# Optimization experiments

Measured on AMD Instinct MI355X. Metric: run time of the kernel, lower is better.

Reference implementation:

```python
import jax, jax.numpy as jnp
import numpy as np

H = 768
NH = 12
DH = H // NH  # 64


def setup_inputs() -> dict:
    key = jax.random.key(0)
    ks = jax.random.split(key, 20)
    s = 1.0 / np.sqrt(H)
    def lin(k, din, dout):
        kw, kb = jax.random.split(k)
        W = jax.random.uniform(kw, (din, dout), jnp.float32, -s, s)
        b = jax.random.uniform(kb, (dout,), jnp.float32, -s, s)
        return W, b
    Wq, bq = lin(ks[0], H, H)
    Wk, bk = lin(ks[1], H, H)
    Wv, bv = lin(ks[2], H, H)
    Wt, bt = lin(ks[3], H, H)
    Wi, bi = lin(ks[4], H, H)
    W1, b1 = lin(ks[5], H, H)
    W2, b2 = lin(ks[6], H, 1)
    text = jax.random.normal(ks[7], (8, 64, H), jnp.float32)
    image = jax.random.normal(ks[8], (8, 197, H), jnp.float32)
    return dict(text=text, image=image, Wq=Wq, bq=bq, Wk=Wk, bk=bk, Wv=Wv, bv=bv,
                Wt=Wt, bt=bt, Wi=Wi, bi=bi, W1=W1, b1=b1, W2=W2, b2=b2)


def reference(text, image, Wq, bq, Wk, bk, Wv, bv, Wt, bt, Wi, bi, W1, b1, W2, b2):
    bsz, t_len, _ = text.shape
    i_len = image.shape[1]
    # relevance gate MLP on broadcast product
    text_emb = text @ Wt + bt          # [b, t, H]
    image_emb = image @ Wi + bi        # [b, i, H]
    rel = text_emb[:, :, None, :] * image_emb[:, None, :, :]  # [b, t, i, H]
    rel = jax.nn.relu(rel @ W1 + b1)
    gate = jax.nn.sigmoid(rel @ W2 + b2)  # [b, t, i, 1]
    gate = gate.reshape(bsz, 1, t_len, i_len)
    # cross-attention
    def heads(x, L):
        return x.reshape(bsz, L, NH, DH).transpose(0, 2, 1, 3)  # [b, h, L, dh]
    q = heads(text @ Wq + bq, t_len)
    k = heads(image @ Wk + bk, i_len)
    v = heads(image @ Wv + bv, i_len)
    scores = jnp.einsum('bhtd,bhid->bhti', q, k) / np.sqrt(DH)
    probs = jax.nn.softmax(scores, axis=-1) * gate   # [b, h, t, i]
    ctx = jnp.einsum('bhti,bhid->bhtd', probs, v)    # [b, h, t, dh]
    return ctx.transpose(0, 2, 1, 3).reshape(bsz, t_len, H)
```

## Files before the change

### kernel.cpp

```cpp
#include <hip/hip_runtime.h>
#include <stdint.h>

#define HD 768
#define NHEADS 12
#define DHEAD 64
#define BATCH 8
#define TLEN 64
#define ILEN 197
#define NPAIRS 100864
#define MTILES 394

typedef __attribute__((ext_vector_type(8))) short short8;
typedef __attribute__((ext_vector_type(4))) float f32x4;

__device__ __forceinline__ short f2bf(float x) {
    union { float f; uint32_t u; } v; v.f = x;
    uint32_t r = v.u + 0x7FFFu + ((v.u >> 16) & 1u);
    return (short)(r >> 16);
}
__device__ __forceinline__ float bf2f(short s) {
    union { uint32_t u; float f; } v; v.u = ((uint32_t)(unsigned short)s) << 16;
    return v.f;
}
__device__ __forceinline__ void gll16(const void* g, void* l) {
    __builtin_amdgcn_global_load_lds(
        (const __attribute__((address_space(1))) unsigned int*)g,
        (__attribute__((address_space(3))) unsigned int*)l, 16, 0, 0);
}

__global__ __launch_bounds__(256) void prep_weights(
    const float* __restrict__ Wq, const float* __restrict__ Wk,
    const float* __restrict__ Wv, const float* __restrict__ Wt,
    const float* __restrict__ Wi, const float* __restrict__ W1,
    short* __restrict__ W5s, short* __restrict__ W1Bs)
{
    __shared__ float tile[64][65];
    int bx = blockIdx.x;
    int tid = threadIdx.x;
    if (bx >= 720) {
        int idx = bx - 720;
        int pn = idx / 12, kt = idx - pn * 12;
        int c = tid;
        int j = pn * 256 + c;
        char* dst = (char*)W1Bs + (size_t)idx * 32768 + c * 128;
        int swz = (c & 7) << 4;
#pragma unroll
        for (int kg = 0; kg < 8; ++kg) {
            short8 o;
#pragma unroll
            for (int e = 0; e < 8; ++e)
                o[e] = f2bf(W1[(size_t)(kt * 64 + kg * 8 + e) * HD + j]);
            *(short8*)(dst + ((kg * 16) ^ swz)) = o;
        }
        return;
    }
    int seg = bx / 144, ti = bx - seg * 144;
    const float* src = (seg == 0) ? Wt : (seg == 1) ? Wq : (seg == 2) ? Wi
                     : (seg == 3) ? Wk : Wv;
    int kt = ti / 12, ntile = ti - kt * 12;
#pragma unroll
    for (int pass = 0; pass < 16; ++pass) {
        int idx = pass * 256 + tid;
        int kk = idx >> 6, nn = idx & 63;
        tile[kk][nn] = src[(size_t)(kt * 64 + kk) * HD + ntile * 64 + nn];
    }
    __syncthreads();
    size_t base = ((size_t)(seg * 12 + ntile) * 12 + kt) * 8192;
#pragma unroll
    for (int pass = 0; pass < 16; ++pass) {
        int idx = pass * 256 + tid;
        int col = idx >> 6, kloc = idx & 63;
        float x = tile[kloc][col];
        short h = f2bf(x);
        short lw = f2bf(x - bf2f(h));
        int sidx = (col * 64 + kloc) ^ ((col & 7) << 3);
        W5s[base + sidx] = h;
        W5s[base + 4096 + sidx] = lw;
    }
}

__global__ __launch_bounds__(256, 1) void proj_kernel(
    const float* __restrict__ X, int M,
    const short* __restrict__ W5s, int segbase,
    const float* __restrict__ bias0, const float* __restrict__ bias1,
    const float* __restrict__ bias2,
    float* __restrict__ out0, float* __restrict__ out1, float* __restrict__ out2)
{
    __shared__ __align__(16) short Bs[2][8192];
    int tid = threadIdx.x;
    int l = tid & 63, w = tid >> 6;
    int lo = l & 15, grp = l >> 4;
    int y = blockIdx.y;
    int segl = y / 12, ntile = y - segl * 12;
    int seg = segbase + segl;
    const char* wsrc = (const char*)W5s + (size_t)((seg * 12 + ntile) * 12) * 16384;
    {
        const char* s = wsrc + w * 4096 + l * 16;
        char* d = (char*)&Bs[0][0] + w * 4096;
        gll16(s, d); gll16(s + 1024, d + 1024);
        gll16(s + 2048, d + 2048); gll16(s + 3072, d + 3072);
    }
    int arow = blockIdx.x * 64 + w * 16 + lo;
    bool aok = arow < M;
    const float* xrow = X + (size_t)(aok ? arow : 0) * HD;
    short8 ah[24], al[24];
#pragma unroll
    for (int kc = 0; kc < 24; ++kc) {
        int kb = kc * 32 + grp * 8;
        float4 xa = {0.f, 0.f, 0.f, 0.f}, xb = {0.f, 0.f, 0.f, 0.f};
        if (aok) { xa = *(const float4*)(xrow + kb); xb = *(const float4*)(xrow + kb + 4); }
        float xs[8] = {xa.x, xa.y, xa.z, xa.w, xb.x, xb.y, xb.z, xb.w};
#pragma unroll
        for (int e = 0; e < 8; ++e) {
            short hh = f2bf(xs[e]);
            ah[kc][e] = hh;
            al[kc][e] = f2bf(xs[e] - bf2f(hh));
        }
    }
    __syncthreads();

    f32x4 acc[4];
    f32x4 z4 = {0.f, 0.f, 0.f, 0.f};
#pragma unroll
    for (int js = 0; js < 4; ++js) acc[js] = z4;

#pragma unroll
    for (int kk = 0; kk < 12; ++kk) {
        const short* buf = &Bs[kk & 1][0];
        if (kk < 11) {
            const char* s = wsrc + (size_t)(kk + 1) * 16384 + w * 4096 + l * 16;
            char* d = (char*)&Bs[(kk + 1) & 1][0] + w * 4096;
            gll16(s, d); gll16(s + 1024, d + 1024);
            gll16(s + 2048, d + 2048); gll16(s + 3072, d + 3072);
            asm volatile("s_waitcnt vmcnt(4)" ::: "memory");
        } else {
            asm volatile("s_waitcnt vmcnt(0)" ::: "memory");
        }
        __builtin_amdgcn_s_barrier();
        asm volatile("" ::: "memory");
#pragma unroll
        for (int js = 0; js < 4; ++js) {
            int col = js * 16 + lo;
            int base = col * 64;
            int sw = (col & 7) << 3;
#pragma unroll
            for (int kcl = 0; kcl < 2; ++kcl) {
                int idx = (base + kcl * 32 + grp * 8) ^ sw;
                short8 bh = *(const short8*)&buf[idx];
                short8 bl = *(const short8*)&buf[4096 + idx];
                int kc = kk * 2 + kcl;
                acc[js] = __builtin_amdgcn_mfma_f32_16x16x32_bf16(ah[kc], bh, acc[js], 0, 0, 0);
                acc[js] = __builtin_amdgcn_mfma_f32_16x16x32_bf16(ah[kc], bl, acc[js], 0, 0, 0);
                acc[js] = __builtin_amdgcn_mfma_f32_16x16x32_bf16(al[kc], bh, acc[js], 0, 0, 0);
            }
        }
        asm volatile("s_waitcnt lgkmcnt(0)" ::: "memory");
        __builtin_amdgcn_s_barrier();
        asm volatile("" ::: "memory");
    }
    const float* bp = (segl == 0) ? bias0 : (segl == 1) ? bias1 : bias2;
    float* op = (segl == 0) ? out0 : (segl == 1) ? out1 : out2;
#pragma unroll
    for (int js = 0; js < 4; ++js) {
        int cc = ntile * 64 + js * 16 + lo;
        float bvv = bp[cc];
#pragma unroll
        for (int r = 0; r < 4; ++r) {
            int orow = blockIdx.x * 64 + w * 16 + grp * 4 + r;
            if (orow < M) op[(size_t)orow * HD + cc] = acc[js][r] + bvv;
        }
    }
}

__global__ __launch_bounds__(256) void build_a(
    const float* __restrict__ te, const float* __restrict__ ie,
    short* __restrict__ As, int mstart)
{
    int bx = blockIdx.x;
    int m_l = bx / 12, kt = bx - m_l * 12;
    int tid = threadIdx.x;
    int p = (mstart + m_l) * 256 + tid;
    int b = p / 12608; int rr = p - b * 12608;
    int t = rr / 197;  int i = rr - t * 197;
    const float* tp = te + (size_t)(b * 64 + t) * HD + kt * 64;
    const float* ip = ie + (size_t)(b * 197 + i) * HD + kt * 64;
    char* dst = (char*)As + ((size_t)(m_l * 12 + kt) * 32768) + tid * 128;
    int swz = (tid & 7) << 4;
#pragma unroll
    for (int kg = 0; kg < 8; ++kg) {
        float4 xa = *(const float4*)(ip + kg * 8);
        float4 xb = *(const float4*)(ip + kg * 8 + 4);
        float4 ta = *(const float4*)(tp + kg * 8);
        float4 tb = *(const float4*)(tp + kg * 8 + 4);
        short8 o;
        o[0] = f2bf(xa.x * ta.x); o[1] = f2bf(xa.y * ta.y);
        o[2] = f2bf(xa.z * ta.z); o[3] = f2bf(xa.w * ta.w);
        o[4] = f2bf(xb.x * tb.x); o[5] = f2bf(xb.y * tb.y);
        o[6] = f2bf(xb.z * tb.z); o[7] = f2bf(xb.w * tb.w);
        *(short8*)(dst + ((kg * 16) ^ swz)) = o;
    }
}

__global__ __launch_bounds__(512, 2) void gate_gemm(
    const short* __restrict__ As, const short* __restrict__ W1Bs,
    const float* __restrict__ b1, const float* __restrict__ W2,
    float* __restrict__ plg, int mstart)
{
    __shared__ __align__(16) char lds[131072];
    int tid = threadIdx.x;
    int lane = tid & 63, wid = tid >> 6;
    int lo = lane & 15, grp = lane >> 4;
    int wr = wid >> 2, wc = wid & 3;
    int bx0 = blockIdx.x;
    int nwg = gridDim.x;
    int qq = nwg >> 3, rr8 = nwg & 7;
    int xcd = bx0 & 7;
    int logical = (xcd < rr8 ? xcd * (qq + 1) : rr8 * (qq + 1) + (xcd - rr8) * qq)
                + (bx0 >> 3);
    int m_l = logical / 3, pn = logical - m_l * 3;

    const char* Ag = (const char*)As + (size_t)m_l * 12 * 32768;
    const char* Bg = (const char*)W1Bs + (size_t)pn * 12 * 32768;

    {
        gll16(Ag + tid * 16,          lds + tid * 16);
        gll16(Ag + 8192 + tid * 16,   lds + 8192 + tid * 16);
        gll16(Ag + 16384 + tid * 16,  lds + 16384 + tid * 16);
        gll16(Ag + 24576 + tid * 16,  lds + 24576 + tid * 16);
        gll16(Bg + tid * 16,          lds + 65536 + tid * 16);
        gll16(Bg + 8192 + tid * 16,   lds + 65536 + 8192 + tid * 16);
        gll16(Bg + 16384 + tid * 16,  lds + 65536 + 16384 + tid * 16);
        gll16(Bg + 24576 + tid * 16,  lds + 65536 + 24576 + tid * 16);
    }
    asm volatile("s_waitcnt vmcnt(0)" ::: "memory");
    __builtin_amdgcn_s_barrier();
    asm volatile("" ::: "memory");

    f32x4 acc[8][4];
    f32x4 z4 = {0.f, 0.f, 0.f, 0.f};
#pragma unroll
    for (int rt = 0; rt < 8; ++rt)
#pragma unroll
        for (int ct = 0; ct < 4; ++ct) acc[rt][ct] = z4;
    int swz = (lo & 7) << 4;

    for (int kt = 0; kt < 12; ++kt) {
        int par = kt & 1, npar = par ^ 1;
        int aoff = par * 32768;
        int boff = 65536 + par * 32768;
        bool more = kt < 11;
        const char* Aun = Ag + (size_t)(kt + 1) * 32768;
        const char* Bun = Bg + (size_t)(kt + 1) * 32768;
        int dA = npar * 32768, dB = 65536 + npar * 32768;

        short8 bfr[4][2];
#pragma unroll
        for (int q = 0; q < 4; ++q) {
            short8 af[2][2];
#pragma unroll
            for (int i2 = 0; i2 < 2; ++i2) {
                int r = wr * 128 + (2 * q + i2) * 16 + lo;
#pragma unroll
                for (int ks = 0; ks < 2; ++ks)
                    af[i2][ks] = *(const short8*)(lds + aoff + r * 128 + ((ks * 64 + grp * 16) ^ swz));
            }
            if (q == 0) {
#pragma unroll
                for (int ct = 0; ct < 4; ++ct) {
                    int c = wc * 64 + ct * 16 + lo;
#pragma unroll
                    for (int ks = 0; ks < 2; ++ks)
                        bfr[ct][ks] = *(const short8*)(lds + boff + c * 128 + ((ks * 64 + grp * 16) ^ swz));
                }
            }
            if (more) {
                if (q < 2) {
                    gll16(Aun + (size_t)(q * 2) * 8192 + tid * 16,
                          lds + dA + (q * 2) * 8192 + tid * 16);
                    gll16(Aun + (size_t)(q * 2 + 1) * 8192 + tid * 16,
                          lds + dA + (q * 2 + 1) * 8192 + tid * 16);
                } else {
                    gll16(Bun + (size_t)((q - 2) * 2) * 8192 + tid * 16,
                          lds + dB + ((q - 2) * 2) * 8192 + tid * 16);
                    gll16(Bun + (size_t)((q - 2) * 2 + 1) * 8192 + tid * 16,
                          lds + dB + ((q - 2) * 2 + 1) * 8192 + tid * 16);
                }
            }
            asm volatile("" ::: "memory");
            __builtin_amdgcn_s_barrier();
            asm volatile("s_waitcnt lgkmcnt(0)" ::: "memory");
            __builtin_amdgcn_sched_barrier(0);
            __builtin_amdgcn_s_setprio(1);
#pragma unroll
            for (int i2 = 0; i2 < 2; ++i2)
#pragma unroll
                for (int ct = 0; ct < 4; ++ct)
#pragma unroll
                    for (int ks = 0; ks < 2; ++ks)
                        acc[2 * q + i2][ct] = __builtin_amdgcn_mfma_f32_16x16x32_bf16(
                            af[i2][ks], bfr[ct][ks], acc[2 * q + i2][ct], 0, 0, 0);
            __builtin_amdgcn_s_setprio(0);
            if (q == 3) {
                asm volatile("s_waitcnt vmcnt(0)" ::: "memory");
            }
            __builtin_amdgcn_s_barrier();
            asm volatile("" ::: "memory");
        }
    }

    float b1v[4], w2v[4];
#pragma unroll
    for (int ct = 0; ct < 4; ++ct) {
        int j = pn * 256 + wc * 64 + ct * 16 + lo;
        b1v[ct] = b1[j]; w2v[ct] = W2[j];
    }
    float pl[8][4];
#pragma unroll
    for (int rt = 0; rt < 8; ++rt)
#pragma unroll
        for (int r = 0; r < 4; ++r) {
            float s = 0.f;
#pragma unroll
            for (int ct = 0; ct < 4; ++ct)
                s += fmaxf(acc[rt][ct][r] + b1v[ct], 0.f) * w2v[ct];
            pl[rt][r] = s;
        }
#pragma unroll
    for (int msk = 1; msk <= 8; msk <<= 1)
#pragma unroll
        for (int rt = 0; rt < 8; ++rt)
#pragma unroll
            for (int r = 0; r < 4; ++r)
                pl[rt][r] += __shfl_xor(pl[rt][r], msk);

    __syncthreads();
    float* red = (float*)lds;
    if (lo == 0) {
#pragma unroll
        for (int rt = 0; rt < 8; ++rt)
#pragma unroll
            for (int r = 0; r < 4; ++r)
                red[wid * 128 + rt * 16 + grp * 4 + r] = pl[rt][r];
    }
    __syncthreads();
    if (tid < 256) {
        int wr_ = tid >> 7, rl = tid & 127;
        float s = red[(wr_ * 4 + 0) * 128 + rl] + red[(wr_ * 4 + 1) * 128 + rl]
                + red[(wr_ * 4 + 2) * 128 + rl] + red[(wr_ * 4 + 3) * 128 + rl];
        plg[(size_t)pn * NPAIRS + (size_t)(mstart + m_l) * 256 + tid] = s;
    }
}

__global__ __launch_bounds__(256) void gate_fin(
    const float* __restrict__ plg, const float* __restrict__ b2,
    float* __restrict__ gateb)
{
    int idx = blockIdx.x * 256 + threadIdx.x;
    if (idx < NPAIRS) {
        float s = plg[idx] + plg[NPAIRS + idx] + plg[2 * NPAIRS + idx] + b2[0];
        gateb[idx] = 1.f / (1.f + __expf(-s));
    }
}

__global__ __launch_bounds__(256) void attn_kernel(
    const float* __restrict__ q, const float* __restrict__ k,
    const float* __restrict__ v, const float* __restrict__ gate,
    float* __restrict__ out)
{
    __shared__ float k_s[ILEN * 65];
    __shared__ float p_s[4][ILEN][4];
    int bx = blockIdx.x;
    int tq = bx & 3;
    int h = (bx >> 2) % NHEADS;
    int b = bx / (4 * NHEADS);
    int tid = threadIdx.x;
    for (int idx = tid; idx < ILEN * DHEAD; idx += 256) {
        int i = idx >> 6, d = idx & 63;
        k_s[i * 65 + d] = k[(size_t)(b * ILEN + i) * HD + h * DHEAD + d];
    }
    __syncthreads();

    int l = tid & 63, w = tid >> 6;
    int tbase = tq * 16 + w * 4;

    for (int tt = 0; tt < 4; ++tt) {
        int t = tbase + tt;
        float qv = q[(size_t)(b * 64 + t) * HD + h * DHEAD + l];
        float s0 = 0.f, s1 = 0.f, s2 = 0.f, s3 = 0.f;
        int i0 = l, i1 = 64 + l, i2 = 128 + l;
        int i3c = (192 + l < ILEN) ? 192 + l : 0;
        for (int d = 0; d < 64; ++d) {
            float qd = __shfl(qv, d);
            s0 += qd * k_s[i0 * 65 + d];
            s1 += qd * k_s[i1 * 65 + d];
            s2 += qd * k_s[i2 * 65 + d];
            s3 += qd * k_s[i3c * 65 + d];
        }
        float sc[4] = {s0, s1, s2, s3};
        float m = -3.0e38f;
#pragma unroll
        for (int rep = 0; rep < 4; ++rep) {
            int i = rep * 64 + l;
            sc[rep] = (i < ILEN) ? sc[rep] * 0.125f : -3.0e38f;
            m = fmaxf(m, sc[rep]);
        }
        for (int mask = 32; mask >= 1; mask >>= 1) m = fmaxf(m, __shfl_xor(m, mask));
        float sum = 0.f;
#pragma unroll
        for (int rep = 0; rep < 4; ++rep) {
            float e = __expf(sc[rep] - m);
            sc[rep] = e;
            sum += e;
        }
        for (int mask = 32; mask >= 1; mask >>= 1) sum += __shfl_xor(sum, mask);
        float inv = 1.f / sum;
        const float* grow = gate + (size_t)(b * 64 + t) * ILEN;
#pragma unroll
        for (int rep = 0; rep < 4; ++rep) {
            int i = rep * 64 + l;
            if (i < ILEN) p_s[w][i][tt] = sc[rep] * inv * grow[i];
        }
    }

    float ctx[4] = {0.f, 0.f, 0.f, 0.f};
    const float* vbase = v + (size_t)(b * ILEN) * HD + h * DHEAD + l;
#pragma unroll 4
    for (int i = 0; i < ILEN; ++i) {
        float vv = vbase[(size_t)i * HD];
        float4 p4 = *(const float4*)&p_s[w][i][0];
        ctx[0] += p4.x * vv;
        ctx[1] += p4.y * vv;
        ctx[2] += p4.z * vv;
        ctx[3] += p4.w * vv;
    }
#pragma unroll
    for (int tt = 0; tt < 4; ++tt)
        out[(size_t)(b * 64 + tbase + tt) * HD + h * DHEAD + l] = ctx[tt];
}

extern "C" void kernel_launch(void* const* d_in, const int* in_sizes, int n_in,
                              void* d_out, int out_size, void* d_ws, size_t ws_size,
                              hipStream_t stream)
{
    const float* text  = (const float*)d_in[0];
    const float* image = (const float*)d_in[1];
    const float* Wq = (const float*)d_in[2];
    const float* bq = (const float*)d_in[3];
    const float* Wk = (const float*)d_in[4];
    const float* bk = (const float*)d_in[5];
    const float* Wv = (const float*)d_in[6];
    const float* bv = (const float*)d_in[7];
    const float* Wt = (const float*)d_in[8];
    const float* bt = (const float*)d_in[9];
    const float* Wi = (const float*)d_in[10];
    const float* bi = (const float*)d_in[11];
    const float* W1 = (const float*)d_in[12];
    const float* b1 = (const float*)d_in[13];
    const float* W2 = (const float*)d_in[14];
    const float* b2 = (const float*)d_in[15];
    float* out = (float*)d_out;

    char* ws = (char*)d_ws;
    size_t off = 0;
    auto carve = [&](size_t bytes) -> void* {
        void* p = (void*)(ws + off);
        off += (bytes + 255) & ~(size_t)255;
        return p;
    };
    short* W5s  = (short*)carve((size_t)5 * 144 * 8192 * 2);
    short* W1Bs = (short*)carve((size_t)36 * 32768);
    float* te    = (float*)carve((size_t)512 * 768 * 4);
    float* qb    = (float*)carve((size_t)512 * 768 * 4);
    float* ieb   = (float*)carve((size_t)1576 * 768 * 4);
    float* kb    = (float*)carve((size_t)1576 * 768 * 4);
    float* vb    = (float*)carve((size_t)1576 * 768 * 4);
    float* gateb = (float*)carve((size_t)NPAIRS * 4);
    float* plg   = (float*)carve((size_t)3 * NPAIRS * 4);

    size_t per_m = (size_t)12 * 32768;
    size_t avail = (ws_size > off) ? (ws_size - off) : 0;
    int stripe = (int)(avail / per_m);
    if (stripe > MTILES) stripe = MTILES;
    if (stripe < 1) stripe = 1;
    short* As = (short*)(ws + off);
    int nst = (MTILES + stripe - 1) / stripe;

    hipLaunchKernelGGL(prep_weights, dim3(756), dim3(256), 0, stream,
                       Wq, Wk, Wv, Wt, Wi, W1, W5s, W1Bs);
    hipLaunchKernelGGL(proj_kernel, dim3(8, 24), dim3(256), 0, stream,
                       text, 512, W5s, 0, bt, bq, (const float*)nullptr,
                       te, qb, (float*)nullptr);
    hipLaunchKernelGGL(proj_kernel, dim3(25, 36), dim3(256), 0, stream,
                       image, 1576, W5s, 2, bi, bk, bv,
                       ieb, kb, vb);
    for (int s = 0; s < nst; ++s) {
        int m0 = s * stripe;
        int mc = (MTILES - m0 < stripe) ? (MTILES - m0) : stripe;
        hipLaunchKernelGGL(build_a, dim3(mc * 12), dim3(256), 0, stream,
                           te, ieb, As, m0);
        hipLaunchKernelGGL(gate_gemm, dim3(mc * 3), dim3(512), 0, stream,
                           As, W1Bs, b1, W2, plg, m0);
    }
    hipLaunchKernelGGL(gate_fin, dim3((NPAIRS + 255) / 256), dim3(256), 0, stream,
                       plg, b2, gateb);
    hipLaunchKernelGGL(attn_kernel, dim3(BATCH * NHEADS * 4), dim3(256), 0, stream,
                       qb, kb, vb, gateb, out);
}
```

Baseline: 346.6 us.

## Retile gate GEMM to 192-wide N and triple-buffer A with one barrier per k-step

The gate GEMM's N tile shrinks from 256 to 192 columns, so there are four column blocks per M tile instead of three. The pre-packed W1 layout, the grid size and the partial-logit buffer (now four partial sums added in gate_fin) are all adjusted to match. The k-loop changes from double-buffering with eight barriers per k-tile to triple-buffered A and double-buffered B tiles. It uses explicit vmcnt waits and a single barrier per k-tile, so loads are issued two stages ahead. This aims to cut barrier stalls, improve overlap of loads with MFMA work, and spread more workgroups across CUs, at the cost of larger LDS use (144KB) and a slightly lower MFMA-to-load ratio per block.

```diff
diff --git a/kernel.cpp b/kernel.cpp
--- a/kernel.cpp
+++ b/kernel.cpp
@@ -41,16 +41,18 @@
         int idx = bx - 720;
         int pn = idx / 12, kt = idx - pn * 12;
         int c = tid;
-        int j = pn * 256 + c;
-        char* dst = (char*)W1Bs + (size_t)idx * 32768 + c * 128;
-        int swz = (c & 7) << 4;
-#pragma unroll
-        for (int kg = 0; kg < 8; ++kg) {
-            short8 o;
-#pragma unroll
-            for (int e = 0; e < 8; ++e)
-                o[e] = f2bf(W1[(size_t)(kt * 64 + kg * 8 + e) * HD + j]);
-            *(short8*)(dst + ((kg * 16) ^ swz)) = o;
+        if (c < 192) {
+            int j = pn * 192 + c;
+            char* dst = (char*)W1Bs + (size_t)idx * 24576 + c * 128;
+            int swz = (c & 7) << 4;
+#pragma unroll
+            for (int kg = 0; kg < 8; ++kg) {
+                short8 o;
+#pragma unroll
+                for (int e = 0; e < 8; ++e)
+                    o[e] = f2bf(W1[(size_t)(kt * 64 + kg * 8 + e) * HD + j]);
+                *(short8*)(dst + ((kg * 16) ^ swz)) = o;
+            }
         }
         return;
     }
@@ -206,7 +208,7 @@
     const float* __restrict__ b1, const float* __restrict__ W2,
     float* __restrict__ plg, int mstart)
 {
-    __shared__ __align__(16) char lds[131072];
+    __shared__ __align__(16) char lds[147456];
     int tid = threadIdx.x;
     int lane = tid & 63, wid = tid >> 6;
     int lo = lane & 15, grp = lane >> 4;
@@ -217,43 +219,51 @@
     int xcd = bx0 & 7;
     int logical = (xcd < rr8 ? xcd * (qq + 1) : rr8 * (qq + 1) + (xcd - rr8) * qq)
                 + (bx0 >> 3);
-    int m_l = logical / 3, pn = logical - m_l * 3;
+    int m_l = logical >> 2, pn = logical & 3;
 
     const char* Ag = (const char*)As + (size_t)m_l * 12 * 32768;
-    const char* Bg = (const char*)W1Bs + (size_t)pn * 12 * 32768;
-
-    {
-        gll16(Ag + tid * 16,          lds + tid * 16);
-        gll16(Ag + 8192 + tid * 16,   lds + 8192 + tid * 16);
-        gll16(Ag + 16384 + tid * 16,  lds + 16384 + tid * 16);
-        gll16(Ag + 24576 + tid * 16,  lds + 24576 + tid * 16);
-        gll16(Bg + tid * 16,          lds + 65536 + tid * 16);
-        gll16(Bg + 8192 + tid * 16,   lds + 65536 + 8192 + tid * 16);
-        gll16(Bg + 16384 + tid * 16,  lds + 65536 + 16384 + tid * 16);
-        gll16(Bg + 24576 + tid * 16,  lds + 65536 + 24576 + tid * 16);
-    }
-    asm volatile("s_waitcnt vmcnt(0)" ::: "memory");
-    __builtin_amdgcn_s_barrier();
-    asm volatile("" ::: "memory");
-
-    f32x4 acc[8][4];
+    const char* Bg = (const char*)W1Bs + (size_t)pn * 12 * 24576;
+
+    auto stageA = [&](int t) {
+        const char* s = Ag + (size_t)t * 32768 + tid * 16;
+        char* d = lds + (t % 3) * 32768 + tid * 16;
+        gll16(s, d); gll16(s + 8192, d + 8192);
+        gll16(s + 16384, d + 16384); gll16(s + 24576, d + 24576);
+    };
+    auto stageB = [&](int t) {
+        const char* s = Bg + (size_t)t * 24576 + tid * 16;
+        char* d = lds + 98304 + (t & 1) * 24576 + tid * 16;
+        gll16(s, d); gll16(s + 8192, d + 8192); gll16(s + 16384, d + 16384);
+    };
+    stageB(0); stageA(0); stageB(1); stageA(1);
+
+    f32x4 acc[8][3];
     f32x4 z4 = {0.f, 0.f, 0.f, 0.f};
 #pragma unroll
     for (int rt = 0; rt < 8; ++rt)
 #pragma unroll
-        for (int ct = 0; ct < 4; ++ct) acc[rt][ct] = z4;
+        for (int ct = 0; ct < 3; ++ct) acc[rt][ct] = z4;
     int swz = (lo & 7) << 4;
 
     for (int kt = 0; kt < 12; ++kt) {
-        int par = kt & 1, npar = par ^ 1;
-        int aoff = par * 32768;
-        int boff = 65536 + par * 32768;
-        bool more = kt < 11;
-        const char* Aun = Ag + (size_t)(kt + 1) * 32768;
-        const char* Bun = Bg + (size_t)(kt + 1) * 32768;
-        int dA = npar * 32768, dB = 65536 + npar * 32768;
-
-        short8 bfr[4][2];
+        if (kt == 0)       asm volatile("s_waitcnt vmcnt(7)" ::: "memory");
+        else if (kt == 11) asm volatile("s_waitcnt vmcnt(0)" ::: "memory");
+        else               asm volatile("s_waitcnt vmcnt(4)" ::: "memory");
+        __builtin_amdgcn_s_barrier();
+        asm volatile("" ::: "memory");
+        if (kt >= 1 && kt + 1 < 12) stageB(kt + 1);
+        if (kt + 2 < 12)            stageA(kt + 2);
+
+        int aoff = (kt % 3) * 32768;
+        int boff = 98304 + (kt & 1) * 24576;
+        short8 bfr[3][2];
+#pragma unroll
+        for (int ct = 0; ct < 3; ++ct) {
+            int c = wc * 48 + ct * 16 + lo;
+#pragma unroll
+            for (int ks = 0; ks < 2; ++ks)
+                bfr[ct][ks] = *(const short8*)(lds + boff + c * 128 + ((ks * 64 + grp * 16) ^ swz));
+        }
 #pragma unroll
         for (int q = 0; q < 4; ++q) {
             short8 af[2][2];
@@ -264,54 +274,23 @@
                 for (int ks = 0; ks < 2; ++ks)
                     af[i2][ks] = *(const short8*)(lds + aoff + r * 128 + ((ks * 64 + grp * 16) ^ swz));
             }
-            if (q == 0) {
-#pragma unroll
-                for (int ct = 0; ct < 4; ++ct) {
-                    int c = wc * 64 + ct * 16 + lo;
-#pragma unroll
-                    for (int ks = 0; ks < 2; ++ks)
-                        bfr[ct][ks] = *(const short8*)(lds + boff + c * 128 + ((ks * 64 + grp * 16) ^ swz));
-                }
-            }
-            if (more) {
-                if (q < 2) {
-                    gll16(Aun + (size_t)(q * 2) * 8192 + tid * 16,
-                          lds + dA + (q * 2) * 8192 + tid * 16);
-                    gll16(Aun + (size_t)(q * 2 + 1) * 8192 + tid * 16,
-                          lds + dA + (q * 2 + 1) * 8192 + tid * 16);
-                } else {
-                    gll16(Bun + (size_t)((q - 2) * 2) * 8192 + tid * 16,
-                          lds + dB + ((q - 2) * 2) * 8192 + tid * 16);
-                    gll16(Bun + (size_t)((q - 2) * 2 + 1) * 8192 + tid * 16,
-                          lds + dB + ((q - 2) * 2 + 1) * 8192 + tid * 16);
-                }
-            }
-            asm volatile("" ::: "memory");
-            __builtin_amdgcn_s_barrier();
-            asm volatile("s_waitcnt lgkmcnt(0)" ::: "memory");
-            __builtin_amdgcn_sched_barrier(0);
             __builtin_amdgcn_s_setprio(1);
 #pragma unroll
             for (int i2 = 0; i2 < 2; ++i2)
 #pragma unroll
-                for (int ct = 0; ct < 4; ++ct)
+                for (int ct = 0; ct < 3; ++ct)
 #pragma unroll
                     for (int ks = 0; ks < 2; ++ks)
                         acc[2 * q + i2][ct] = __builtin_amdgcn_mfma_f32_16x16x32_bf16(
                             af[i2][ks], bfr[ct][ks], acc[2 * q + i2][ct], 0, 0, 0);
             __builtin_amdgcn_s_setprio(0);
-            if (q == 3) {
-                asm volatile("s_waitcnt vmcnt(0)" ::: "memory");
-            }
-            __builtin_amdgcn_s_barrier();
-            asm volatile("" ::: "memory");
-        }
-    }
-
-    float b1v[4], w2v[4];
-#pragma unroll
-    for (int ct = 0; ct < 4; ++ct) {
-        int j = pn * 256 + wc * 64 + ct * 16 + lo;
+        }
+    }
+
+    float b1v[3], w2v[3];
+#pragma unroll
+    for (int ct = 0; ct < 3; ++ct) {
+        int j = pn * 192 + wc * 48 + ct * 16 + lo;
         b1v[ct] = b1[j]; w2v[ct] = W2[j];
     }
     float pl[8][4];
@@ -321,7 +300,7 @@
         for (int r = 0; r < 4; ++r) {
             float s = 0.f;
 #pragma unroll
-            for (int ct = 0; ct < 4; ++ct)
+            for (int ct = 0; ct < 3; ++ct)
                 s += fmaxf(acc[rt][ct][r] + b1v[ct], 0.f) * w2v[ct];
             pl[rt][r] = s;
         }
@@ -357,7 +336,8 @@
 {
     int idx = blockIdx.x * 256 + threadIdx.x;
     if (idx < NPAIRS) {
-        float s = plg[idx] + plg[NPAIRS + idx] + plg[2 * NPAIRS + idx] + b2[0];
+        float s = plg[idx] + plg[NPAIRS + idx] + plg[2 * NPAIRS + idx]
+                + plg[3 * NPAIRS + idx] + b2[0];
         gateb[idx] = 1.f / (1.f + __expf(-s));
     }
 }
@@ -468,14 +448,14 @@
         return p;
     };
     short* W5s  = (short*)carve((size_t)5 * 144 * 8192 * 2);
-    short* W1Bs = (short*)carve((size_t)36 * 32768);
+    short* W1Bs = (short*)carve((size_t)48 * 24576);
     float* te    = (float*)carve((size_t)512 * 768 * 4);
     float* qb    = (float*)carve((size_t)512 * 768 * 4);
     float* ieb   = (float*)carve((size_t)1576 * 768 * 4);
     float* kb    = (float*)carve((size_t)1576 * 768 * 4);
     float* vb    = (float*)carve((size_t)1576 * 768 * 4);
     float* gateb = (float*)carve((size_t)NPAIRS * 4);
-    float* plg   = (float*)carve((size_t)3 * NPAIRS * 4);
+    float* plg   = (float*)carve((size_t)4 * NPAIRS * 4);
 
     size_t per_m = (size_t)12 * 32768;
     size_t avail = (ws_size > off) ? (ws_size - off) : 0;
@@ -485,7 +465,7 @@
     short* As = (short*)(ws + off);
     int nst = (MTILES + stripe - 1) / stripe;
 
-    hipLaunchKernelGGL(prep_weights, dim3(756), dim3(256), 0, stream,
+    hipLaunchKernelGGL(prep_weights, dim3(768), dim3(256), 0, stream,
                        Wq, Wk, Wv, Wt, Wi, W1, W5s, W1Bs);
     hipLaunchKernelGGL(proj_kernel, dim3(8, 24), dim3(256), 0, stream,
                        text, 512, W5s, 0, bt, bq, (const float*)nullptr,
@@ -498,7 +478,7 @@
         int mc = (MTILES - m0 < stripe) ? (MTILES - m0) : stripe;
         hipLaunchKernelGGL(build_a, dim3(mc * 12), dim3(256), 0, stream,
                            te, ieb, As, m0);
-        hipLaunchKernelGGL(gate_gemm, dim3(mc * 3), dim3(512), 0, stream,
+        hipLaunchKernelGGL(gate_gemm, dim3(mc * 4), dim3(512), 0, stream,
                            As, W1Bs, b1, W2, plg, m0);
     }
     hipLaunchKernelGGL(gate_fin, dim3((NPAIRS + 255) / 256), dim3(256), 0, stream,
```

New measurement: 361.7 us. 1.04x slower.

## Fuse relevance-product A-tile construction into gate GEMM and drop striped launches

Applied to the files above, without the earlier changes.

Removes the separate build_a kernel and its bf16 staging buffer. Each gate_gemm block now builds its own A tile in LDS from the text and image embeddings (elementwise product, then bf16 conversion), for the next K step, while the MFMAs for the current step run. This avoids writing and re-reading roughly 150MB of intermediate A data and the striped launch loop. In exchange, the fp32 embeddings are re-read three times (once per N-tile block), the per-q barriers are replaced by one barrier per K step, and the A construction uses plain vector global loads instead of direct-to-LDS loads, so latency overlap depends on the compiler's scheduling.

```diff
diff --git a/kernel.cpp b/kernel.cpp
--- a/kernel.cpp
+++ b/kernel.cpp
@@ -172,39 +172,10 @@
     }
 }
 
-__global__ __launch_bounds__(256) void build_a(
+__global__ __launch_bounds__(512, 2) void gate_gemm(
     const float* __restrict__ te, const float* __restrict__ ie,
-    short* __restrict__ As, int mstart)
-{
-    int bx = blockIdx.x;
-    int m_l = bx / 12, kt = bx - m_l * 12;
-    int tid = threadIdx.x;
-    int p = (mstart + m_l) * 256 + tid;
-    int b = p / 12608; int rr = p - b * 12608;
-    int t = rr / 197;  int i = rr - t * 197;
-    const float* tp = te + (size_t)(b * 64 + t) * HD + kt * 64;
-    const float* ip = ie + (size_t)(b * 197 + i) * HD + kt * 64;
-    char* dst = (char*)As + ((size_t)(m_l * 12 + kt) * 32768) + tid * 128;
-    int swz = (tid & 7) << 4;
-#pragma unroll
-    for (int kg = 0; kg < 8; ++kg) {
-        float4 xa = *(const float4*)(ip + kg * 8);
-        float4 xb = *(const float4*)(ip + kg * 8 + 4);
-        float4 ta = *(const float4*)(tp + kg * 8);
-        float4 tb = *(const float4*)(tp + kg * 8 + 4);
-        short8 o;
-        o[0] = f2bf(xa.x * ta.x); o[1] = f2bf(xa.y * ta.y);
-        o[2] = f2bf(xa.z * ta.z); o[3] = f2bf(xa.w * ta.w);
-        o[4] = f2bf(xb.x * tb.x); o[5] = f2bf(xb.y * tb.y);
-        o[6] = f2bf(xb.z * tb.z); o[7] = f2bf(xb.w * tb.w);
-        *(short8*)(dst + ((kg * 16) ^ swz)) = o;
-    }
-}
-
-__global__ __launch_bounds__(512, 2) void gate_gemm(
-    const short* __restrict__ As, const short* __restrict__ W1Bs,
-    const float* __restrict__ b1, const float* __restrict__ W2,
-    float* __restrict__ plg, int mstart)
+    const short* __restrict__ W1Bs, const float* __restrict__ b1,
+    const float* __restrict__ W2, float* __restrict__ plg)
 {
     __shared__ __align__(16) char lds[131072];
     int tid = threadIdx.x;
@@ -219,20 +190,47 @@
                 + (bx0 >> 3);
     int m_l = logical / 3, pn = logical - m_l * 3;
 
-    const char* Ag = (const char*)As + (size_t)m_l * 12 * 32768;
     const char* Bg = (const char*)W1Bs + (size_t)pn * 12 * 32768;
 
+    int crow = wid * 32 + (lane >> 1);
+    int ckh  = lane & 1;
     {
-        gll16(Ag + tid * 16,          lds + tid * 16);
-        gll16(Ag + 8192 + tid * 16,   lds + 8192 + tid * 16);
-        gll16(Ag + 16384 + tid * 16,  lds + 16384 + tid * 16);
-        gll16(Ag + 24576 + tid * 16,  lds + 24576 + tid * 16);
-        gll16(Bg + tid * 16,          lds + 65536 + tid * 16);
-        gll16(Bg + 8192 + tid * 16,   lds + 65536 + 8192 + tid * 16);
-        gll16(Bg + 16384 + tid * 16,  lds + 65536 + 16384 + tid * 16);
-        gll16(Bg + 24576 + tid * 16,  lds + 65536 + 24576 + tid * 16);
-    }
-    asm volatile("s_waitcnt vmcnt(0)" ::: "memory");
+    }
+    int cp = m_l * 256 + crow;
+    int cb = cp / 12608; int crr = cp - cb * 12608;
+    int ct_ = crr / 197; int ci = crr - ct_ * 197;
+    const float* ctp = te + (size_t)(cb * 64 + ct_) * HD + ckh * 32;
+    const float* cip = ie + (size_t)(cb * 197 + ci) * HD + ckh * 32;
+    int cawz = (crow & 7) << 4;
+    int ckg0 = ckh * 4;
+
+    auto constructA = [&](int t, int par) {
+        const float* tpk = ctp + (size_t)t * 64;
+        const float* ipk = cip + (size_t)t * 64;
+        char* ab = lds + par * 32768 + crow * 128;
+#pragma unroll
+        for (int g = 0; g < 4; ++g) {
+            float4 ta = *(const float4*)(tpk + g * 8);
+            float4 tb = *(const float4*)(tpk + g * 8 + 4);
+            float4 xa = *(const float4*)(ipk + g * 8);
+            float4 xb = *(const float4*)(ipk + g * 8 + 4);
+            short8 o;
+            o[0] = f2bf(xa.x * ta.x); o[1] = f2bf(xa.y * ta.y);
+            o[2] = f2bf(xa.z * ta.z); o[3] = f2bf(xa.w * ta.w);
+            o[4] = f2bf(xb.x * tb.x); o[5] = f2bf(xb.y * tb.y);
+            o[6] = f2bf(xb.z * tb.z); o[7] = f2bf(xb.w * tb.w);
+            *(short8*)(ab + (((ckg0 + g) * 16) ^ cawz)) = o;
+        }
+    };
+
+    constructA(0, 0);
+    {
+        const char* s = Bg + tid * 16;
+        char* d = lds + 65536 + tid * 16;
+        gll16(s, d); gll16(s + 8192, d + 8192);
+        gll16(s + 16384, d + 16384); gll16(s + 24576, d + 24576);
+    }
+    asm volatile("s_waitcnt vmcnt(0) lgkmcnt(0)" ::: "memory");
     __builtin_amdgcn_s_barrier();
     asm volatile("" ::: "memory");
 
@@ -249,11 +247,22 @@
         int aoff = par * 32768;
         int boff = 65536 + par * 32768;
         bool more = kt < 11;
-        const char* Aun = Ag + (size_t)(kt + 1) * 32768;
-        const char* Bun = Bg + (size_t)(kt + 1) * 32768;
-        int dA = npar * 32768, dB = 65536 + npar * 32768;
+
+        if (more) {
+            const char* s = Bg + (size_t)(kt + 1) * 32768 + tid * 16;
+            char* d = lds + 65536 + npar * 32768 + tid * 16;
+            gll16(s, d); gll16(s + 8192, d + 8192);
+            gll16(s + 16384, d + 16384); gll16(s + 24576, d + 24576);
+        }
 
         short8 bfr[4][2];
+#pragma unroll
+        for (int ct = 0; ct < 4; ++ct) {
+            int c = wc * 64 + ct * 16 + lo;
+#pragma unroll
+            for (int ks = 0; ks < 2; ++ks)
+                bfr[ct][ks] = *(const short8*)(lds + boff + c * 128 + ((ks * 64 + grp * 16) ^ swz));
+        }
 #pragma unroll
         for (int q = 0; q < 4; ++q) {
             short8 af[2][2];
@@ -264,32 +273,6 @@
                 for (int ks = 0; ks < 2; ++ks)
                     af[i2][ks] = *(const short8*)(lds + aoff + r * 128 + ((ks * 64 + grp * 16) ^ swz));
             }
-            if (q == 0) {
-#pragma unroll
-                for (int ct = 0; ct < 4; ++ct) {
-                    int c = wc * 64 + ct * 16 + lo;
-#pragma unroll
-                    for (int ks = 0; ks < 2; ++ks)
-                        bfr[ct][ks] = *(const short8*)(lds + boff + c * 128 + ((ks * 64 + grp * 16) ^ swz));
-                }
-            }
-            if (more) {
-                if (q < 2) {
-                    gll16(Aun + (size_t)(q * 2) * 8192 + tid * 16,
-                          lds + dA + (q * 2) * 8192 + tid * 16);
-                    gll16(Aun + (size_t)(q * 2 + 1) * 8192 + tid * 16,
-                          lds + dA + (q * 2 + 1) * 8192 + tid * 16);
-                } else {
-                    gll16(Bun + (size_t)((q - 2) * 2) * 8192 + tid * 16,
-                          lds + dB + ((q - 2) * 2) * 8192 + tid * 16);
-                    gll16(Bun + (size_t)((q - 2) * 2 + 1) * 8192 + tid * 16,
-                          lds + dB + ((q - 2) * 2 + 1) * 8192 + tid * 16);
-                }
-            }
-            asm volatile("" ::: "memory");
-            __builtin_amdgcn_s_barrier();
-            asm volatile("s_waitcnt lgkmcnt(0)" ::: "memory");
-            __builtin_amdgcn_sched_barrier(0);
             __builtin_amdgcn_s_setprio(1);
 #pragma unroll
             for (int i2 = 0; i2 < 2; ++i2)
@@ -300,12 +283,13 @@
                         acc[2 * q + i2][ct] = __builtin_amdgcn_mfma_f32_16x16x32_bf16(
                             af[i2][ks], bfr[ct][ks], acc[2 * q + i2][ct], 0, 0, 0);
             __builtin_amdgcn_s_setprio(0);
-            if (q == 3) {
-                asm volatile("s_waitcnt vmcnt(0)" ::: "memory");
-            }
-            __builtin_amdgcn_s_barrier();
-            asm volatile("" ::: "memory");
-        }
+        }
+
+        if (more) constructA(kt + 1, npar);
+
+        asm volatile("s_waitcnt vmcnt(0) lgkmcnt(0)" ::: "memory");
+        __builtin_amdgcn_s_barrier();
+        asm volatile("" ::: "memory");
     }
 
     float b1v[4], w2v[4];
@@ -347,7 +331,7 @@
         int wr_ = tid >> 7, rl = tid & 127;
         float s = red[(wr_ * 4 + 0) * 128 + rl] + red[(wr_ * 4 + 1) * 128 + rl]
                 + red[(wr_ * 4 + 2) * 128 + rl] + red[(wr_ * 4 + 3) * 128 + rl];
-        plg[(size_t)pn * NPAIRS + (size_t)(mstart + m_l) * 256 + tid] = s;
+        plg[(size_t)pn * NPAIRS + (size_t)m_l * 256 + tid] = s;
     }
 }
 
@@ -477,14 +461,6 @@
     float* gateb = (float*)carve((size_t)NPAIRS * 4);
     float* plg   = (float*)carve((size_t)3 * NPAIRS * 4);
 
-    size_t per_m = (size_t)12 * 32768;
-    size_t avail = (ws_size > off) ? (ws_size - off) : 0;
-    int stripe = (int)(avail / per_m);
-    if (stripe > MTILES) stripe = MTILES;
-    if (stripe < 1) stripe = 1;
-    short* As = (short*)(ws + off);
-    int nst = (MTILES + stripe - 1) / stripe;
-
     hipLaunchKernelGGL(prep_weights, dim3(756), dim3(256), 0, stream,
                        Wq, Wk, Wv, Wt, Wi, W1, W5s, W1Bs);
     hipLaunchKernelGGL(proj_kernel, dim3(8, 24), dim3(256), 0, stream,
@@ -493,14 +469,8 @@
     hipLaunchKernelGGL(proj_kernel, dim3(25, 36), dim3(256), 0, stream,
                        image, 1576, W5s, 2, bi, bk, bv,
                        ieb, kb, vb);
-    for (int s = 0; s < nst; ++s) {
-        int m0 = s * stripe;
-        int mc = (MTILES - m0 < stripe) ? (MTILES - m0) : stripe;
-        hipLaunchKernelGGL(build_a, dim3(mc * 12), dim3(256), 0, stream,
-                           te, ieb, As, m0);
-        hipLaunchKernelGGL(gate_gemm, dim3(mc * 3), dim3(512), 0, stream,
-                           As, W1Bs, b1, W2, plg, m0);
-    }
+    hipLaunchKernelGGL(gate_gemm, dim3(MTILES * 3), dim3(512), 0, stream,
+                       te, ieb, W1Bs, b1, W2, plg);
     hipLaunchKernelGGL(gate_fin, dim3((NPAIRS + 255) / 256), dim3(256), 0, stream,
                        plg, b2, gateb);
     hipLaunchKernelGGL(attn_kernel, dim3(BATCH * NHEADS * 4), dim3(256), 0, stream,
```

Measured after the change: 397.7 us. 14.7% more time.

## Split K-tiles into half-slabs for finer-grained gate GEMM pipelining

Applied to the files above, without the earlier changes.

Changes the bf16 A/W1 tile layout from 128-byte rows to two 64-byte-row half-K slabs with a new XOR swizzle, updating producers (prep_weights, build_a) and the consumer GEMM to match. The gate GEMM now waits only for the first half-slab before computing and overlaps per-half loads with partial vmcnt waits, so compute on ks=0 can start while ks=1 is still arriving. build_a now stages inputs through shared memory for coalesced loads and uses packed bf16 conversion instructions. The extra LDS staging and syncs in build_a add overhead, and the finer wait counts must match the number of outstanding loads exactly.

```diff
diff --git a/kernel.cpp b/kernel.cpp
--- a/kernel.cpp
+++ b/kernel.cpp
@@ -22,6 +22,11 @@
     union { uint32_t u; float f; } v; v.u = ((uint32_t)(unsigned short)s) << 16;
     return v.f;
 }
+__device__ __forceinline__ uint32_t cvtpk(float lo, float hi) {
+    uint32_t r;
+    asm("v_cvt_pk_bf16_f32 %0, %1, %2" : "=v"(r) : "v"(lo), "v"(hi));
+    return r;
+}
 __device__ __forceinline__ void gll16(const void* g, void* l) {
     __builtin_amdgcn_global_load_lds(
         (const __attribute__((address_space(1))) unsigned int*)g,
@@ -42,15 +47,19 @@
         int pn = idx / 12, kt = idx - pn * 12;
         int c = tid;
         int j = pn * 256 + c;
-        char* dst = (char*)W1Bs + (size_t)idx * 32768 + c * 128;
-        int swz = (c & 7) << 4;
-#pragma unroll
-        for (int kg = 0; kg < 8; ++kg) {
-            short8 o;
-#pragma unroll
-            for (int e = 0; e < 8; ++e)
-                o[e] = f2bf(W1[(size_t)(kt * 64 + kg * 8 + e) * HD + j]);
-            *(short8*)(dst + ((kg * 16) ^ swz)) = o;
+        char* chunk = (char*)W1Bs + (size_t)idx * 32768;
+        int f = (c >> 1) & 3;
+#pragma unroll
+        for (int ks = 0; ks < 2; ++ks) {
+            char* dst = chunk + ks * 16384 + c * 64;
+#pragma unroll
+            for (int g = 0; g < 4; ++g) {
+                short8 o;
+#pragma unroll
+                for (int e = 0; e < 8; ++e)
+                    o[e] = f2bf(W1[(size_t)(kt * 64 + ks * 32 + g * 8 + e) * HD + j]);
+                *(short8*)(dst + ((g * 16) ^ (f << 4))) = o;
+            }
         }
         return;
     }
@@ -176,28 +185,44 @@
     const float* __restrict__ te, const float* __restrict__ ie,
     short* __restrict__ As, int mstart)
 {
+    __shared__ float raw[2][256][68];
+    __shared__ int offs[2][256];
     int bx = blockIdx.x;
     int m_l = bx / 12, kt = bx - m_l * 12;
     int tid = threadIdx.x;
-    int p = (mstart + m_l) * 256 + tid;
-    int b = p / 12608; int rr = p - b * 12608;
-    int t = rr / 197;  int i = rr - t * 197;
-    const float* tp = te + (size_t)(b * 64 + t) * HD + kt * 64;
-    const float* ip = ie + (size_t)(b * 197 + i) * HD + kt * 64;
-    char* dst = (char*)As + ((size_t)(m_l * 12 + kt) * 32768) + tid * 128;
-    int swz = (tid & 7) << 4;
-#pragma unroll
-    for (int kg = 0; kg < 8; ++kg) {
-        float4 xa = *(const float4*)(ip + kg * 8);
-        float4 xb = *(const float4*)(ip + kg * 8 + 4);
-        float4 ta = *(const float4*)(tp + kg * 8);
-        float4 tb = *(const float4*)(tp + kg * 8 + 4);
-        short8 o;
-        o[0] = f2bf(xa.x * ta.x); o[1] = f2bf(xa.y * ta.y);
-        o[2] = f2bf(xa.z * ta.z); o[3] = f2bf(xa.w * ta.w);
-        o[4] = f2bf(xb.x * tb.x); o[5] = f2bf(xb.y * tb.y);
-        o[6] = f2bf(xb.z * tb.z); o[7] = f2bf(xb.w * tb.w);
-        *(short8*)(dst + ((kg * 16) ^ swz)) = o;
+    {
+        int p = (mstart + m_l) * 256 + tid;
+        int b = p / 12608; int rr = p - b * 12608;
+        int t = rr / 197;  int i = rr - t * 197;
+        offs[0][tid] = (b * 197 + i) * HD + kt * 64;
+        offs[1][tid] = (b * 64 + t) * HD + kt * 64;
+    }
+    __syncthreads();
+    for (int it = 0; it < 16; ++it) {
+        int idx = it * 256 + tid;
+        int row = idx >> 4, f4 = idx & 15;
+        *(float4*)&raw[0][row][f4 * 4] = *(const float4*)(ie + offs[0][row] + f4 * 4);
+        *(float4*)&raw[1][row][f4 * 4] = *(const float4*)(te + offs[1][row] + f4 * 4);
+    }
+    __syncthreads();
+    char* chunk = (char*)As + (size_t)(m_l * 12 + kt) * 32768;
+    int f = (tid >> 1) & 3;
+#pragma unroll
+    for (int ks = 0; ks < 2; ++ks) {
+        uint32_t o[16];
+#pragma unroll
+        for (int g = 0; g < 8; ++g) {
+            float4 x  = *(const float4*)&raw[0][tid][ks * 32 + g * 4];
+            float4 t4 = *(const float4*)&raw[1][tid][ks * 32 + g * 4];
+            o[g * 2]     = cvtpk(x.x * t4.x, x.y * t4.y);
+            o[g * 2 + 1] = cvtpk(x.z * t4.z, x.w * t4.w);
+        }
+        char* dst = chunk + ks * 16384 + tid * 64;
+#pragma unroll
+        for (int g2 = 0; g2 < 4; ++g2) {
+            uint4 v = {o[4 * g2], o[4 * g2 + 1], o[4 * g2 + 2], o[4 * g2 + 3]};
+            *(uint4*)(dst + ((g2 * 16) ^ (f << 4))) = v;
+        }
     }
 }
 
@@ -222,17 +247,18 @@
     const char* Ag = (const char*)As + (size_t)m_l * 12 * 32768;
     const char* Bg = (const char*)W1Bs + (size_t)pn * 12 * 32768;
 
-    {
-        gll16(Ag + tid * 16,          lds + tid * 16);
-        gll16(Ag + 8192 + tid * 16,   lds + 8192 + tid * 16);
-        gll16(Ag + 16384 + tid * 16,  lds + 16384 + tid * 16);
-        gll16(Ag + 24576 + tid * 16,  lds + 24576 + tid * 16);
-        gll16(Bg + tid * 16,          lds + 65536 + tid * 16);
-        gll16(Bg + 8192 + tid * 16,   lds + 65536 + 8192 + tid * 16);
-        gll16(Bg + 16384 + tid * 16,  lds + 65536 + 16384 + tid * 16);
-        gll16(Bg + 24576 + tid * 16,  lds + 65536 + 24576 + tid * 16);
-    }
-    asm volatile("s_waitcnt vmcnt(0)" ::: "memory");
+    auto stageA = [&](int t, int ks) {
+        const char* s = Ag + (size_t)t * 32768 + ks * 16384 + tid * 16;
+        char* d = lds + (t & 1) * 32768 + ks * 16384 + tid * 16;
+        gll16(s, d); gll16(s + 8192, d + 8192);
+    };
+    auto stageB = [&](int t, int ks) {
+        const char* s = Bg + (size_t)t * 32768 + ks * 16384 + tid * 16;
+        char* d = lds + 65536 + (t & 1) * 32768 + ks * 16384 + tid * 16;
+        gll16(s, d); gll16(s + 8192, d + 8192);
+    };
+    stageA(0, 0); stageA(0, 1); stageB(0, 0); stageB(0, 1);
+    asm volatile("s_waitcnt vmcnt(2)" ::: "memory");
     __builtin_amdgcn_s_barrier();
     asm volatile("" ::: "memory");
 
@@ -242,66 +268,55 @@
     for (int rt = 0; rt < 8; ++rt)
 #pragma unroll
         for (int ct = 0; ct < 4; ++ct) acc[rt][ct] = z4;
-    int swz = (lo & 7) << 4;
 
     for (int kt = 0; kt < 12; ++kt) {
-        int par = kt & 1, npar = par ^ 1;
+        int par = kt & 1;
         int aoff = par * 32768;
         int boff = 65536 + par * 32768;
         bool more = kt < 11;
-        const char* Aun = Ag + (size_t)(kt + 1) * 32768;
-        const char* Bun = Bg + (size_t)(kt + 1) * 32768;
-        int dA = npar * 32768, dB = 65536 + npar * 32768;
-
-        short8 bfr[4][2];
-#pragma unroll
-        for (int q = 0; q < 4; ++q) {
-            short8 af[2][2];
-#pragma unroll
-            for (int i2 = 0; i2 < 2; ++i2) {
-                int r = wr * 128 + (2 * q + i2) * 16 + lo;
-#pragma unroll
-                for (int ks = 0; ks < 2; ++ks)
-                    af[i2][ks] = *(const short8*)(lds + aoff + r * 128 + ((ks * 64 + grp * 16) ^ swz));
-            }
-            if (q == 0) {
+        short8 bfr[4], af[4];
+
+#pragma unroll
+        for (int ph = 0; ph < 4; ++ph) {
+            int ksp = ph >> 1;
+            int rh  = ph & 1;
+            if (rh == 0) {
 #pragma unroll
                 for (int ct = 0; ct < 4; ++ct) {
                     int c = wc * 64 + ct * 16 + lo;
-#pragma unroll
-                    for (int ks = 0; ks < 2; ++ks)
-                        bfr[ct][ks] = *(const short8*)(lds + boff + c * 128 + ((ks * 64 + grp * 16) ^ swz));
+                    bfr[ct] = *(const short8*)(lds + boff + ksp * 16384 + c * 64
+                                + ((grp * 16) ^ (((c >> 1) & 3) << 4)));
                 }
             }
+#pragma unroll
+            for (int j = 0; j < 4; ++j) {
+                int r = wr * 128 + (rh * 4 + j) * 16 + lo;
+                af[j] = *(const short8*)(lds + aoff + ksp * 16384 + r * 64
+                            + ((grp * 16) ^ (((r >> 1) & 3) << 4)));
+            }
             if (more) {
-                if (q < 2) {
-                    gll16(Aun + (size_t)(q * 2) * 8192 + tid * 16,
-                          lds + dA + (q * 2) * 8192 + tid * 16);
-                    gll16(Aun + (size_t)(q * 2 + 1) * 8192 + tid * 16,
-                          lds + dA + (q * 2 + 1) * 8192 + tid * 16);
-                } else {
-                    gll16(Bun + (size_t)((q - 2) * 2) * 8192 + tid * 16,
-                          lds + dB + ((q - 2) * 2) * 8192 + tid * 16);
-                    gll16(Bun + (size_t)((q - 2) * 2 + 1) * 8192 + tid * 16,
-                          lds + dB + ((q - 2) * 2 + 1) * 8192 + tid * 16);
-                }
+                if (ph == 0)      stageA(kt + 1, 0);
+                else if (ph == 1) stageA(kt + 1, 1);
+                else if (ph == 2) stageB(kt + 1, 0);
+                else              stageB(kt + 1, 1);
             }
-            asm volatile("" ::: "memory");
             __builtin_amdgcn_s_barrier();
             asm volatile("s_waitcnt lgkmcnt(0)" ::: "memory");
             __builtin_amdgcn_sched_barrier(0);
             __builtin_amdgcn_s_setprio(1);
 #pragma unroll
-            for (int i2 = 0; i2 < 2; ++i2)
+            for (int j = 0; j < 4; ++j)
 #pragma unroll
                 for (int ct = 0; ct < 4; ++ct)
-#pragma unroll
-                    for (int ks = 0; ks < 2; ++ks)
-                        acc[2 * q + i2][ct] = __builtin_amdgcn_mfma_f32_16x16x32_bf16(
-                            af[i2][ks], bfr[ct][ks], acc[2 * q + i2][ct], 0, 0, 0);
+                    acc[rh * 4 + j][ct] = __builtin_amdgcn_mfma_f32_16x16x32_bf16(
+                        af[j], bfr[ct], acc[rh * 4 + j][ct], 0, 0, 0);
             __builtin_amdgcn_s_setprio(0);
-            if (q == 3) {
-                asm volatile("s_waitcnt vmcnt(0)" ::: "memory");
+            if (ph == 1) {
+                if (more) asm volatile("s_waitcnt vmcnt(4)" ::: "memory");
+                else      asm volatile("s_waitcnt vmcnt(0)" ::: "memory");
+            } else if (ph == 3) {
+                if (more) asm volatile("s_waitcnt vmcnt(2)" ::: "memory");
+                else      asm volatile("s_waitcnt vmcnt(0)" ::: "memory");
             }
             __builtin_amdgcn_s_barrier();
             asm volatile("" ::: "memory");
```

New measurement: 353.6 us. 2.0% more time.
